# Kernel tuning notes

Measured on AMD Instinct MI355X. Metric: run time of the kernel, lower is better.

## Reference

```python
import jax, jax.numpy as jnp
import numpy as np

N, D_IN, WID, LAT, DPD, H, N_SEG = 131072, 128, 512, 512, 128, 8, 256


def cumulative_segment_mean(data, segment_ids):
    # prefix mean that resets at each new (sorted) segment id
    n = data.shape[0]
    idx = jnp.arange(n)
    seg_start = jnp.concatenate([jnp.ones((1,), bool), segment_ids[1:] != segment_ids[:-1]])
    # index of the first element of each token's segment
    start_idx = jax.lax.associative_scan(jnp.maximum, jnp.where(seg_start, idx, 0))
    cs = jnp.cumsum(data, axis=0)
    base = jnp.where((start_idx > 0)[:, None], cs[jnp.maximum(start_idx - 1, 0)], jnp.zeros((), data.dtype))
    count = (idx - start_idx + 1).astype(data.dtype)[:, None]
    return (cs - base) / count


def setup_inputs() -> dict:
    key = jax.random.key(0)
    ks = jax.random.split(key, 12)
    he = lambda k, sh: jax.random.normal(k, sh, jnp.float32) * np.sqrt(2.0 / sh[0]).astype(np.float32)
    inputs = jax.random.normal(ks[0], (N, D_IN), jnp.float32)
    segment_ids = jnp.sort(jax.random.randint(ks[1], (N,), 0, N_SEG, dtype=jnp.int64))
    return {
        "inputs": inputs,
        "segment_ids": segment_ids,
        "W1": he(ks[2], (D_IN, WID)), "b1": jnp.zeros((WID,), jnp.float32),
        "W2": he(ks[3], (WID, WID)), "b2": jnp.zeros((WID,), jnp.float32),
        "W3": he(ks[4], (WID, LAT)), "b3": jnp.zeros((LAT,), jnp.float32),
        "Wr": he(ks[5], (LAT, LAT)), "br": jnp.zeros((LAT,), jnp.float32),
        "W_k": he(ks[6], (LAT + D_IN, DPD * H)),
        "W_q": jax.random.normal(ks[7], (H, DPD), jnp.float32) * 0.05,
    }


def reference(inputs, segment_ids, W1, b1, W2, b2, W3, b3, Wr, br, W_k, W_q):
    relu = jax.nn.relu
    h = relu(inputs @ W1 + b1)          # psi layer 1
    h = relu(h @ W2 + b2)               # psi layer 2
    encoded = relu(h @ W3 + b3)         # psi latent projection
    agg = cumulative_segment_mean(encoded, segment_ids)
    agg = relu(agg @ Wr + br)           # rho
    combined = jnp.concatenate([inputs, agg], axis=-1)   # [N, D_IN+LAT]
    keys = (combined @ W_k).reshape(inputs.shape[0], H, DPD)  # split+stack heads
    preattn = jnp.einsum('nhd,hd->nh', keys, W_q) / jnp.sqrt(jnp.float32(DPD))
    return preattn
```

## Files before the change

kernel.cpp:

```cpp
#include <hip/hip_runtime.h>
#include <hip/hip_bf16.h>
#include <stdint.h>

typedef unsigned short ushortT;
typedef __bf16 bf16x8 __attribute__((ext_vector_type(8)));
typedef float f32x4 __attribute__((ext_vector_type(4)));

#define N_TOK 131072
#define NSEG  256
#define RSPL  8

__device__ __forceinline__ uint32_t f2bf(float f) {
  union { float f; uint32_t u; } c; c.f = f;
  uint32_t u = c.u;
  u += 0x7fffu + ((u >> 16) & 1u);
  return u >> 16;
}
__device__ __forceinline__ float bf2f(uint32_t b) {
  union { uint32_t u; float f; } c; c.u = b << 16;
  return c.f;
}

__device__ __forceinline__ void gload_lds16(const void* g, void* l) {
  __builtin_amdgcn_global_load_lds(
      (const __attribute__((address_space(1))) void*)g,
      (__attribute__((address_space(3))) void*)l, 16, 0, 0);
}


__global__ void transpose_bf16_kernel(const float* __restrict__ W, ushortT* __restrict__ WT,
                                      int Kd, int Nd) {
  int i = blockIdx.x * 256 + threadIdx.x;
  if (i < Kd * Nd) {
    int n = i / Kd, k = i % Kd;
    WT[i] = (ushortT)f2bf(W[(size_t)k * Nd + n]);
  }
}

__global__ void weff_kernel(const float* __restrict__ Wk, const float* __restrict__ Wq,
                            ushortT* __restrict__ weffT) {
  const int c = blockIdx.x;
  const int lane = threadIdx.x;
  const float rs = 0.08838834764831845f;
#pragma unroll
  for (int h = 0; h < 8; ++h) {
    float acc = Wk[(size_t)c * 1024 + h * 128 + lane] * Wq[h * 128 + lane]
              + Wk[(size_t)c * 1024 + h * 128 + 64 + lane] * Wq[h * 128 + 64 + lane];
#pragma unroll
    for (int off = 32; off >= 1; off >>= 1) acc += __shfl_xor(acc, off, 64);
    if (lane == 0) {
      weffT[h * 640 + c]       = (ushortT)f2bf(acc * rs);
      weffT[(h + 8) * 640 + c] = 0;
    }
  }
}

__global__ void seg_bounds_kernel(const int* __restrict__ seg, int* __restrict__ gbnd) {
  const int s = (int)threadIdx.x + (int)blockIdx.x * 512;
  if (s > NSEG) return;
  int lo = 0, hi = N_TOK;
  while (lo < hi) { int m = (lo + hi) >> 1; if (seg[m] < s) lo = m + 1; else hi = m; }
  gbnd[s] = lo;
}


template <int K, bool RELU, bool BIAS, bool XF32>
__global__ __launch_bounds__(256, 3)
void gemm_m97_kernel(const void* __restrict__ Av, const ushortT* __restrict__ BT,
                     const float* __restrict__ bias, ushortT* __restrict__ C) {
  __shared__ ushortT lA[128 * 64];
  __shared__ ushortT lB[128 * 64];
  constexpr int NT = K / 64;

  const int nwg  = (int)gridDim.x;
  const int cpx  = nwg >> 3;
  const int flat = (int)blockIdx.x;
  const int swz  = (flat & 7) * cpx + (flat >> 3);
  const int bm   = swz >> 2;
  const int bn   = swz & 3;

  const int t = (int)threadIdx.x;
  const int w = t >> 6, lane = t & 63;
  const int wm = w >> 1, wn = w & 1;
  const int q = lane >> 4, lr = lane & 15;

  const int srow = t >> 3;
  const int slc  = (t & 7) ^ (srow & 7);

  const ushortT* Ab = nullptr;
  const float*   Xf = nullptr;
  if (XF32) Xf = (const float*)Av + (size_t)(bm * 128 + srow) * 128 + slc * 8;
  else      Ab = (const ushortT*)Av + (size_t)(bm * 128 + srow) * K + slc * 8;
  const ushortT* Bg = BT + (size_t)(bn * 128 + srow) * K + slc * 8;

  f32x4 acc[4][4];
#pragma unroll
  for (int i = 0; i < 4; ++i)
#pragma unroll
    for (int j = 0; j < 4; ++j) acc[i][j] = 0.f;

  const int cc0 = (q ^ (lr & 7)) << 4;
  const int cc1 = ((4 + q) ^ (lr & 7)) << 4;
  const char* lAc = (const char*)lA;
  const char* lBc = (const char*)lB;

#pragma unroll 1
  for (int kt = 0; kt < NT; ++kt) {
    {
      const ushortT* src = Bg + kt * 64;
#pragma unroll
      for (int j = 0; j < 4; ++j)
        gload_lds16(src + (size_t)j * 32 * K, (char*)lB + j * 4096 + t * 16);
    }
    if (XF32) {
      const float* src = Xf + kt * 64;
#pragma unroll
      for (int j = 0; j < 4; ++j) {
        const float4 v0 = *(const float4*)(src + (size_t)j * 32 * 128);
        const float4 v1 = *(const float4*)(src + (size_t)j * 32 * 128 + 4);
        uint4 pk;
        pk.x = f2bf(v0.x) | (f2bf(v0.y) << 16);
        pk.y = f2bf(v0.z) | (f2bf(v0.w) << 16);
        pk.z = f2bf(v1.x) | (f2bf(v1.y) << 16);
        pk.w = f2bf(v1.z) | (f2bf(v1.w) << 16);
        *(uint4*)((char*)lA + j * 4096 + t * 16) = pk;
      }
    } else {
      const ushortT* src = Ab + kt * 64;
#pragma unroll
      for (int j = 0; j < 4; ++j)
        gload_lds16(src + (size_t)j * 32 * K, (char*)lA + j * 4096 + t * 16);
    }
    __syncthreads();

    bf16x8 a0[4], a1[4], b0[4], b1[4];
#pragma unroll
    for (int m = 0; m < 4; ++m) {
      const int ro = (wm * 64 + m * 16 + lr) * 128;
      a0[m] = *(const bf16x8*)(lAc + ro + cc0);
      a1[m] = *(const bf16x8*)(lAc + ro + cc1);
    }
#pragma unroll
    for (int n = 0; n < 4; ++n) {
      const int ro = (wn * 64 + n * 16 + lr) * 128;
      b0[n] = *(const bf16x8*)(lBc + ro + cc0);
      b1[n] = *(const bf16x8*)(lBc + ro + cc1);
    }

    __builtin_amdgcn_s_setprio(1);
#pragma unroll
    for (int n = 0; n < 4; ++n)
#pragma unroll
      for (int m = 0; m < 4; ++m)
        acc[m][n] = __builtin_amdgcn_mfma_f32_16x16x32_bf16(a0[m], b0[n], acc[m][n], 0, 0, 0);
#pragma unroll
    for (int n = 0; n < 4; ++n)
#pragma unroll
      for (int m = 0; m < 4; ++m)
        acc[m][n] = __builtin_amdgcn_mfma_f32_16x16x32_bf16(a1[m], b1[n], acc[m][n], 0, 0, 0);
    __builtin_amdgcn_s_setprio(0);

    __syncthreads();
  }

  const int row0 = bm * 128 + wm * 64 + q * 4;
  const int col0 = bn * 128 + wn * 64 + lr;
#pragma unroll
  for (int n = 0; n < 4; ++n) {
    const int col = col0 + n * 16;
    const float bvv = BIAS ? bias[col] : 0.f;
#pragma unroll
    for (int m = 0; m < 4; ++m) {
#pragma unroll
      for (int r = 0; r < 4; ++r) {
        float v = acc[m][n][r] + bvv;
        if (RELU) v = fmaxf(v, 0.f);
        C[(size_t)(row0 + m * 16 + r) * 512 + col] = (ushortT)f2bf(v);
      }
    }
  }
}


__global__ __launch_bounds__(256)
void seg_sum_kernel(const ushortT* __restrict__ z, const int* __restrict__ gbnd,
                    float* __restrict__ part, int c0, int rows) {
  const int s  = (int)blockIdx.x >> 3;
  const int rg = (int)blockIdx.x & 7;
  const int t  = (int)threadIdx.x;

  const int gb0 = gbnd[s], gb1 = gbnd[s + 1];
  int beg = gb0 > c0 ? gb0 : c0;
  int end = gb1 < c0 + rows ? gb1 : c0 + rows;
  int len = end - beg; if (len < 0) len = 0;
  const int r0 = beg + ((len * rg) >> 3);
  const int r1 = beg + ((len * (rg + 1)) >> 3);

  float a0 = 0.f, a1 = 0.f;
  const uint32_t* __restrict__ zp = (const uint32_t*)z;
  int r = r0;
  for (; r + 8 <= r1; r += 8) {
    uint32_t v[8];
#pragma unroll
    for (int i = 0; i < 8; ++i) v[i] = zp[(size_t)(r + i - c0) * 256 + t];
#pragma unroll
    for (int i = 0; i < 8; ++i) { a0 += bf2f(v[i] & 0xffffu); a1 += bf2f(v[i] >> 16); }
  }
  for (; r < r1; ++r) {
    const uint32_t v = zp[(size_t)(r - c0) * 256 + t];
    a0 += bf2f(v & 0xffffu); a1 += bf2f(v >> 16);
  }
  float2 pv; pv.x = a0; pv.y = a1;
  ((float2*)part)[(s * 8 + rg) * 256 + t] = pv;
}

__global__ __launch_bounds__(256)
void seg_scan2_kernel(const ushortT* __restrict__ z, ushortT* __restrict__ gout,
                      const int* __restrict__ gbnd, const float* __restrict__ br,
                      const float* __restrict__ part,
                      const float* __restrict__ cin, float* __restrict__ cout,
                      int c0, int rows) {
  const int s  = (int)blockIdx.x >> 3;
  const int rg = (int)blockIdx.x & 7;
  const int t  = (int)threadIdx.x;

  const int gb0 = gbnd[s], gb1 = gbnd[s + 1];
  int beg = gb0 > c0 ? gb0 : c0;
  int end = gb1 < c0 + rows ? gb1 : c0 + rows;
  int len = end - beg; if (len < 0) len = 0;
  const int r0 = beg + ((len * rg) >> 3);
  const int r1 = beg + ((len * (rg + 1)) >> 3);

  const float2 cv = ((const float2*)cin)[s * 256 + t];
  float a0 = cv.x, a1 = cv.y;
  for (int q2 = 0; q2 < rg; ++q2) {
    const float2 pv = ((const float2*)part)[(s * 8 + q2) * 256 + t];
    a0 += pv.x; a1 += pv.y;
  }
  int cb = c0 - gb0; if (cb < 0) cb = 0;
  const int seglen = gb1 - gb0; if (cb > seglen) cb = seglen;
  const int cnt0 = cb + (r0 - beg);

  const float b0 = br[2 * t], b1v = br[2 * t + 1];
  const uint32_t* __restrict__ zp = (const uint32_t*)z;
  uint32_t* __restrict__ gp = (uint32_t*)gout;

  int r = r0;
  for (; r + 8 <= r1; r += 8) {
    uint32_t v[8];
#pragma unroll
    for (int i = 0; i < 8; ++i) v[i] = zp[(size_t)(r + i - c0) * 256 + t];
#pragma unroll
    for (int i = 0; i < 8; ++i) {
      a0 += bf2f(v[i] & 0xffffu);
      a1 += bf2f(v[i] >> 16);
      const float inv = __builtin_amdgcn_rcpf((float)(cnt0 + (r + i) - r0 + 1));
      const float g0 = fmaxf(fmaf(a0, inv, b0), 0.f);
      const float g1 = fmaxf(fmaf(a1, inv, b1v), 0.f);
      gp[(size_t)(r + i - c0) * 256 + t] = f2bf(g0) | (f2bf(g1) << 16);
    }
  }
  for (; r < r1; ++r) {
    const uint32_t v = zp[(size_t)(r - c0) * 256 + t];
    a0 += bf2f(v & 0xffffu);
    a1 += bf2f(v >> 16);
    const float inv = __builtin_amdgcn_rcpf((float)(cnt0 + r - r0 + 1));
    const float g0 = fmaxf(fmaf(a0, inv, b0), 0.f);
    const float g1 = fmaxf(fmaf(a1, inv, b1v), 0.f);
    gp[(size_t)(r - c0) * 256 + t] = f2bf(g0) | (f2bf(g1) << 16);
  }

  if (rg == 7) {
    float2 co; co.x = a0; co.y = a1;
    ((float2*)cout)[s * 256 + t] = co;
  }
}


__global__ __launch_bounds__(256)
void final_mfma_kernel(const float* __restrict__ X, const ushortT* __restrict__ g,
                       const ushortT* __restrict__ weffT, float* __restrict__ out) {
  __shared__ char lw[16 * 1296];
  const int t = (int)threadIdx.x;

#pragma unroll
  for (int i = 0; i < 5; ++i) {
    const int idx = i * 256 + t;
    const int row = idx / 80, c = idx % 80;
    *(uint4*)(lw + row * 1296 + c * 16) =
        *(const uint4*)((const char*)weffT + row * 1280 + c * 16);
  }
  __syncthreads();

  const int wv = t >> 6, lane = t & 63;
  const int q = lane >> 4, lr = lane & 15;
  const int rbase = (int)blockIdx.x * 128 + wv * 32;

  f32x4 acc[2];
  acc[0] = 0.f; acc[1] = 0.f;

#pragma unroll
  for (int kk = 0; kk < 20; ++kk) {
    const bf16x8 b = *(const bf16x8*)(lw + lr * 1296 + kk * 64 + q * 16);
#pragma unroll
    for (int mt = 0; mt < 2; ++mt) {
      const int row = rbase + mt * 16 + lr;
      union { ushortT u[8]; bf16x8 v; } a;
      if (kk < 4) {
        const float* xr = X + (size_t)row * 128 + kk * 32 + q * 8;
        const float4 v0 = *(const float4*)xr;
        const float4 v1 = *(const float4*)(xr + 4);
        a.u[0] = (ushortT)f2bf(v0.x); a.u[1] = (ushortT)f2bf(v0.y);
        a.u[2] = (ushortT)f2bf(v0.z); a.u[3] = (ushortT)f2bf(v0.w);
        a.u[4] = (ushortT)f2bf(v1.x); a.u[5] = (ushortT)f2bf(v1.y);
        a.u[6] = (ushortT)f2bf(v1.z); a.u[7] = (ushortT)f2bf(v1.w);
      } else {
        a.v = *(const bf16x8*)(g + (size_t)row * 512 + (kk - 4) * 32 + q * 8);
      }
      acc[mt] = __builtin_amdgcn_mfma_f32_16x16x32_bf16(a.v, b, acc[mt], 0, 0, 0);
    }
  }

  if (lr < 8) {
#pragma unroll
    for (int mt = 0; mt < 2; ++mt)
#pragma unroll
      for (int r = 0; r < 4; ++r)
        out[(size_t)(rbase + mt * 16 + q * 4 + r) * 8 + lr] = acc[mt][r];
  }
}


extern "C" void kernel_launch(void* const* d_in, const int* in_sizes, int n_in,
                              void* d_out, int out_size, void* d_ws, size_t ws_size,
                              hipStream_t stream) {
  const float* X  = (const float*)d_in[0];
  const int*   sg = (const int*)d_in[1];
  const float* W1 = (const float*)d_in[2];
  const float* b1 = (const float*)d_in[3];
  const float* W2 = (const float*)d_in[4];
  const float* b2 = (const float*)d_in[5];
  const float* W3 = (const float*)d_in[6];
  const float* b3 = (const float*)d_in[7];
  const float* Wr = (const float*)d_in[8];
  const float* br = (const float*)d_in[9];
  const float* Wk = (const float*)d_in[10];
  const float* Wq = (const float*)d_in[11];
  float* out = (float*)d_out;

  const size_t szW1T  = 512 * 128 * 2;
  const size_t szWT   = 512 * 512 * 2;
  const size_t szWeff = 16 * 640 * 2;
  const size_t szPart = (size_t)NSEG * RSPL * 256 * 2 * 4;
  const size_t szCar  = (size_t)NSEG * 256 * 2 * 4;
  const size_t szBnd  = (NSEG + 1) * 4;
  const size_t fixed  = szW1T + 3 * szWT + szWeff + szPart + 2 * szCar + szBnd + 512;

  int CH = 0;
  const int cands[6] = {131072, 65536, 32768, 16384, 8192, 4096};
  for (int i = 0; i < 6; ++i) {
    const size_t need = fixed + 2 * (size_t)cands[i] * 512 * 2;
    if (need <= ws_size) { CH = cands[i]; break; }
  }
  if (CH == 0) CH = 4096;

  char* p = (char*)d_ws;
  ushortT* W1T   = (ushortT*)p; p += szW1T;
  ushortT* W2T   = (ushortT*)p; p += szWT;
  ushortT* W3T   = (ushortT*)p; p += szWT;
  ushortT* WrT   = (ushortT*)p; p += szWT;
  ushortT* weffT = (ushortT*)p; p += szWeff;
  float*   part  = (float*)p;   p += szPart;
  float*   carA  = (float*)p;   p += szCar;
  float*   carB  = (float*)p;   p += szCar;
  int*     gbnd  = (int*)p;     p += (szBnd + 255) & ~255ull;
  ushortT* p1    = (ushortT*)p; p += (size_t)CH * 512 * 2;
  ushortT* p2    = (ushortT*)p;

  transpose_bf16_kernel<<<(512 * 128 + 255) / 256, 256, 0, stream>>>(W1, W1T, 128, 512);
  transpose_bf16_kernel<<<(512 * 512 + 255) / 256, 256, 0, stream>>>(W2, W2T, 512, 512);
  transpose_bf16_kernel<<<(512 * 512 + 255) / 256, 256, 0, stream>>>(W3, W3T, 512, 512);
  transpose_bf16_kernel<<<(512 * 512 + 255) / 256, 256, 0, stream>>>(Wr, WrT, 512, 512);
  weff_kernel<<<640, 64, 0, stream>>>(Wk, Wq, weffT);
  seg_bounds_kernel<<<1, 512, 0, stream>>>(sg, gbnd);
  hipMemsetAsync(carA, 0, szCar, stream);

  int par = 0;
  for (int c0 = 0; c0 < N_TOK; c0 += CH) {
    const int gG = (CH / 128) * 4;
    float* cin  = par ? carB : carA;
    float* cout = par ? carA : carB;
    gemm_m97_kernel<128, true,  true,  true ><<<gG, 256, 0, stream>>>(X + (size_t)c0 * 128, W1T, b1, p1);
    gemm_m97_kernel<512, true,  true,  false><<<gG, 256, 0, stream>>>(p1, W2T, b2, p2);
    gemm_m97_kernel<512, true,  true,  false><<<gG, 256, 0, stream>>>(p2, W3T, b3, p1);
    gemm_m97_kernel<512, false, false, false><<<gG, 256, 0, stream>>>(p1, WrT, nullptr, p2);
    seg_sum_kernel <<<NSEG * RSPL, 256, 0, stream>>>(p2, gbnd, part, c0, CH);
    seg_scan2_kernel<<<NSEG * RSPL, 256, 0, stream>>>(p2, p1, gbnd, br, part,
                                                      cin, cout, c0, CH);
    final_mfma_kernel<<<CH / 128, 256, 0, stream>>>(X + (size_t)c0 * 128, p1, weffT,
                                                    out + (size_t)c0 * 8);
    par ^= 1;
  }
}
```

Measured before the change: 424.6 us.

## Add triple-buffered 256x128-tile GEMM kernel for the 512-wide layers

Adds a new GEMM kernel that uses a three-slot LDS ring with direct global-to-LDS loads, prefetching two K-tiles ahead and computing each wave's 128x64 sub-tile with bf16 MFMAs. The block tile grows to 256x128 so each block does more MFMA work per staged byte. It runs at one block per CU because of the 144KB of LDS. It replaces the previous kernel for the three K=512 layers and aims to hide global latency and raise operand reuse. The cost is lower occupancy, fewer blocks per launch and more accumulator registers.

```diff
diff --git a/kernel.cpp b/kernel.cpp
--- a/kernel.cpp
+++ b/kernel.cpp
@@ -61,6 +61,119 @@
   int lo = 0, hi = N_TOK;
   while (lo < hi) { int m = (lo + hi) >> 1; if (seg[m] < s) lo = m + 1; else hi = m; }
   gbnd[s] = lo;
+}
+
+
+template <int K, bool RELU, bool BIAS>
+__global__ __launch_bounds__(256, 1)
+void gemm_ring_kernel(const ushortT* __restrict__ A, const ushortT* __restrict__ BT,
+                      const float* __restrict__ bias, ushortT* __restrict__ C) {
+  __shared__ char lds[3 * 49152];
+  constexpr int NT = K / 64;
+
+  const int nwg  = (int)gridDim.x;
+  const int cpx  = nwg >> 3;
+  const int flat = (int)blockIdx.x;
+  const int swz  = (flat & 7) * cpx + (flat >> 3);
+  const int bm   = swz >> 2;
+  const int bn   = swz & 3;
+
+  const int t = (int)threadIdx.x;
+  const int w = t >> 6, lane = t & 63;
+  const int wm = w >> 1, wn = w & 1;
+  const int q = lane >> 4, lr = lane & 15;
+
+  const int srow = t >> 3;
+  const int slc  = (t & 7) ^ (srow & 7);
+  const ushortT* Ag = A  + (size_t)(bm * 256 + srow) * K + slc * 8;
+  const ushortT* Bg = BT + (size_t)(bn * 128 + srow) * K + slc * 8;
+
+  f32x4 acc[8][4];
+#pragma unroll
+  for (int i = 0; i < 8; ++i)
+#pragma unroll
+    for (int j = 0; j < 4; ++j) acc[i][j] = 0.f;
+
+#define STAGE(tile)                                                           \
+  {                                                                           \
+    char* _d = lds + ((tile) % 3) * 49152 + t * 16;                           \
+    const ushortT* _ga = Ag + (size_t)(tile) * 64;                            \
+    _Pragma("unroll")                                                         \
+    for (int _p = 0; _p < 8; ++_p)                                            \
+      gload_lds16(_ga + (size_t)_p * 32 * K, _d + _p * 4096);                 \
+    char* _db = _d + 32768;                                                   \
+    const ushortT* _gb = Bg + (size_t)(tile) * 64;                            \
+    _Pragma("unroll")                                                         \
+    for (int _p = 0; _p < 4; ++_p)                                            \
+      gload_lds16(_gb + (size_t)_p * 32 * K, _db + _p * 4096);                \
+  }
+
+  STAGE(0);
+  if (NT > 1) STAGE(1);
+
+  const int cc0 = (q ^ (lr & 7)) << 4;
+  const int cc1 = ((4 + q) ^ (lr & 7)) << 4;
+  const int aro = (wm * 128 + lr) * 128;
+  const int bro = 32768 + (wn * 64 + lr) * 128;
+
+#pragma unroll 1
+  for (int j = 0; j < NT; ++j) {
+    if (j + 1 < NT) asm volatile("s_waitcnt vmcnt(12)" ::: "memory");
+    else            asm volatile("s_waitcnt vmcnt(0)"  ::: "memory");
+    __builtin_amdgcn_s_barrier();
+    asm volatile("" ::: "memory");
+
+    if (j + 2 < NT) STAGE(j + 2);
+
+    const char* sl = lds + (j % 3) * 49152;
+
+    {
+      bf16x8 a[8], b[4];
+#pragma unroll
+      for (int m = 0; m < 8; ++m) a[m] = *(const bf16x8*)(sl + aro + m * 2048 + cc0);
+#pragma unroll
+      for (int n = 0; n < 4; ++n) b[n] = *(const bf16x8*)(sl + bro + n * 2048 + cc0);
+      __builtin_amdgcn_s_setprio(1);
+#pragma unroll
+      for (int n = 0; n < 4; ++n)
+#pragma unroll
+        for (int m = 0; m < 8; ++m)
+          acc[m][n] = __builtin_amdgcn_mfma_f32_16x16x32_bf16(a[m], b[n], acc[m][n], 0, 0, 0);
+      __builtin_amdgcn_s_setprio(0);
+    }
+    {
+      bf16x8 a[8], b[4];
+#pragma unroll
+      for (int m = 0; m < 8; ++m) a[m] = *(const bf16x8*)(sl + aro + m * 2048 + cc1);
+#pragma unroll
+      for (int n = 0; n < 4; ++n) b[n] = *(const bf16x8*)(sl + bro + n * 2048 + cc1);
+      __builtin_amdgcn_s_setprio(1);
+#pragma unroll
+      for (int n = 0; n < 4; ++n)
+#pragma unroll
+        for (int m = 0; m < 8; ++m)
+          acc[m][n] = __builtin_amdgcn_mfma_f32_16x16x32_bf16(a[m], b[n], acc[m][n], 0, 0, 0);
+      __builtin_amdgcn_s_setprio(0);
+    }
+  }
+#undef STAGE
+
+  const int row0 = bm * 256 + wm * 128 + q * 4;
+  const int col0 = bn * 128 + wn * 64 + lr;
+#pragma unroll
+  for (int n = 0; n < 4; ++n) {
+    const int col = col0 + n * 16;
+    const float bvv = BIAS ? bias[col] : 0.f;
+#pragma unroll
+    for (int m = 0; m < 8; ++m) {
+#pragma unroll
+      for (int r = 0; r < 4; ++r) {
+        float v = acc[m][n][r] + bvv;
+        if (RELU) v = fmaxf(v, 0.f);
+        C[(size_t)(row0 + m * 16 + r) * 512 + col] = (ushortT)f2bf(v);
+      }
+    }
+  }
 }
 
 
@@ -387,13 +500,14 @@
 
   int par = 0;
   for (int c0 = 0; c0 < N_TOK; c0 += CH) {
-    const int gG = (CH / 128) * 4;
+    const int gG1 = (CH / 128) * 4;
+    const int gGR = (CH / 256) * 4;
     float* cin  = par ? carB : carA;
     float* cout = par ? carA : carB;
-    gemm_m97_kernel<128, true,  true,  true ><<<gG, 256, 0, stream>>>(X + (size_t)c0 * 128, W1T, b1, p1);
-    gemm_m97_kernel<512, true,  true,  false><<<gG, 256, 0, stream>>>(p1, W2T, b2, p2);
-    gemm_m97_kernel<512, true,  true,  false><<<gG, 256, 0, stream>>>(p2, W3T, b3, p1);
-    gemm_m97_kernel<512, false, false, false><<<gG, 256, 0, stream>>>(p1, WrT, nullptr, p2);
+    gemm_m97_kernel<128, true, true, true><<<gG1, 256, 0, stream>>>(X + (size_t)c0 * 128, W1T, b1, p1);
+    gemm_ring_kernel<512, true,  true ><<<gGR, 256, 0, stream>>>(p1, W2T, b2, p2);
+    gemm_ring_kernel<512, true,  true ><<<gGR, 256, 0, stream>>>(p2, W3T, b3, p1);
+    gemm_ring_kernel<512, false, false><<<gGR, 256, 0, stream>>>(p1, WrT, nullptr, p2);
     seg_sum_kernel <<<NSEG * RSPL, 256, 0, stream>>>(p2, gbnd, part, c0, CH);
     seg_scan2_kernel<<<NSEG * RSPL, 256, 0, stream>>>(p2, p1, gbnd, br, part,
                                                       cin, cout, c0, CH);
```

New measurement: 489.5 us. 15.3% more time.
